# Performance work log

Hardware: AMD Instinct MI355X
Metric: run time of the kernel (lower is better)

Reference implementation:

```python
import jax, jax.numpy as jnp
import numpy as np

SPACE = 63
STRIDE = 2
TEMP = 0.07
W_CHAR, W_WORD, W_PHRASE, W_IDEA = 1.0, 0.5, 0.1, 0.1


def setup_inputs() -> dict:
    key = jax.random.key(0)
    ks = jax.random.split(key, 6)
    B, S, V, D = 8, 4096, 256, 512
    return {
        "logits": jax.random.normal(ks[0], (B, S, V), jnp.float32),
        "word_preds": jax.random.normal(ks[1], (B, D, S // STRIDE), jnp.float32),
        "char_features": jax.random.normal(ks[2], (B, D, S), jnp.float32),
        "contrastive_2": jax.random.normal(ks[3], (B, 128, 1024), jnp.float32),
        "contrastive_3": jax.random.normal(ks[4], (B, 128, 256), jnp.float32),
        "targets": jax.random.randint(ks[5], (B, S), 0, V, jnp.int32),
        "mask": jnp.ones((B, S), jnp.float32),
    }


def _info_nce(emb, temp=TEMP):
    # emb: (B, dim, L). Anchors = even positions, positives = odd positions.
    B, dim, L = emb.shape
    n_pairs = L // 2
    a = emb[:, :, 0:2 * n_pairs:2].transpose(0, 2, 1).reshape(-1, dim)
    p = emb[:, :, 1:2 * n_pairs:2].transpose(0, 2, 1).reshape(-1, dim)
    a = a / jnp.maximum(jnp.linalg.norm(a, axis=1, keepdims=True), 1e-12)
    p = p / jnp.maximum(jnp.linalg.norm(p, axis=1, keepdims=True), 1e-12)
    logits = (a @ p.T) / temp  # (n, n)
    n = logits.shape[0]
    logp = jax.nn.log_softmax(logits, axis=1)
    idx = jnp.arange(n)
    return -jnp.mean(logp[idx, idx])


def _word_span_loss(word_preds, char_features, targets, stride=STRIDE):
    # Segment-mean over spans between consecutive spaces; MSE vs gathered preds.
    B, D, S = char_features.shape
    Wlen = word_preds.shape[2]
    nseg = S + 2  # segment k in [1, n_spaces-1] = span after the k-th space; last slot = junk
    space = targets == SPACE
    cs = jnp.cumsum(space.astype(jnp.int32), axis=1)  # inclusive space count
    seg = jnp.where(space, nseg - 1, cs)          # non-space chars -> span id
    seg_sp = jnp.where(space, cs, nseg - 1)       # space positions -> their space index k
    t_idx = jnp.arange(S, dtype=jnp.int32)

    def per_batch(feats, seg_b, seg_sp_b):
        sums = jax.ops.segment_sum(feats.T, seg_b, num_segments=nseg)  # (nseg, D)
        cnts = jax.ops.segment_sum(jnp.ones((S,), feats.dtype), seg_b, num_segments=nseg)
        pos = jnp.full((nseg,), S, jnp.int32).at[seg_sp_b].set(t_idx)  # position of k-th space
        return sums, cnts, pos

    sums, cnts, pos = jax.vmap(per_batch)(char_features, seg, seg_sp)
    n_sp = cs[:, -1]  # (B,)
    k = jnp.arange(nseg)[None, :]
    valid = (k >= 1) & (k <= n_sp[:, None] - 1) & (cnts > 0) & ((pos // stride) < Wlen)
    means = jax.lax.stop_gradient(sums / jnp.maximum(cnts, 1.0)[..., None])  # target.detach()
    wp = jnp.clip(pos // stride, 0, Wlen - 1)  # (B, nseg)
    preds = jnp.take_along_axis(word_preds.transpose(0, 2, 1), wp[:, :, None], axis=1)  # (B,nseg,D)
    mse = jnp.mean((preds - means) ** 2, axis=-1)  # per-span F.mse_loss (mean over feat dim)
    tot = jnp.sum(jnp.where(valid, mse, 0.0))
    cnt = jnp.sum(valid).astype(mse.dtype)
    return jnp.where(cnt > 0, tot / jnp.maximum(cnt, 1.0), 0.0)


def reference(logits, word_preds, char_features, contrastive_2, contrastive_3, targets, mask):
    # char CE with mask
    logp = jax.nn.log_softmax(logits, axis=-1)
    ce = -jnp.take_along_axis(logp, targets[..., None].astype(jnp.int32), axis=-1)[..., 0]
    n = jnp.sum(mask)
    char_loss = jnp.where(n > 0, jnp.sum(ce * mask) / jnp.maximum(n, 1.0), jnp.mean(ce))
    word_loss = _word_span_loss(word_preds, char_features, targets)
    phrase_loss = _info_nce(contrastive_2)
    idea_loss = _info_nce(contrastive_3)
    return (W_CHAR * char_loss + W_WORD * word_loss
            + W_PHRASE * phrase_loss + W_IDEA * idea_loss)
```

## Files before the change

### kernel.cpp

```cpp
#include <hip/hip_runtime.h>

#define SPACE_TOK 63
#define INV_T 14.285714285714286f
#define SA_SCALE 20.609929155556595f
#define LN2F 0.6931471805599453f

typedef __attribute__((ext_vector_type(8))) short bf16x8;
typedef __attribute__((ext_vector_type(4))) float f32x4;

#define O_NSP    0
#define O_SPPOS  64
#define O_CECM   131136
#define O_CEM    135232
#define O_CEC    139328
#define O_WPART  143424
#define O_WCNT   159808
#define O_NP2    160832
#define O_NP3    161856
#define O_A2     162304
#define SZ_A2    (4096*128*2)
#define O_P2     (O_A2 + SZ_A2)
#define O_A3     (O_P2 + SZ_A2)
#define SZ_A3    (1024*128*2)
#define O_P3     (O_A3 + SZ_A3)

__device__ inline unsigned short f2bf(float x) {
  union { float f; unsigned int u; } c; c.f = x;
  unsigned int r = c.u + 0x7fffu + ((c.u >> 16) & 1u);
  return (unsigned short)(r >> 16);
}

__device__ void scan_body(char* smem, const int* __restrict__ targets, char* ws, int b) {
  int tid = threadIdx.x;
  int* toks = (int*)smem;
  int* sc   = (int*)(smem + 16384);
  int* n_sp   = (int*)(ws + O_NSP);
  int* sp_pos = (int*)(ws + O_SPPOS);
  const int4* tb4 = (const int4*)(targets + b * 4096);
#pragma unroll
  for (int i = 0; i < 4; ++i) ((int4*)toks)[tid + 256 * i] = tb4[tid + 256 * i];
  __syncthreads();
  int base = tid * 16;
  int cnt = 0;
#pragma unroll
  for (int i = 0; i < 16; ++i) cnt += (toks[base + i] == SPACE_TOK);
  sc[tid] = cnt;
  __syncthreads();
  for (int off = 1; off < 256; off <<= 1) {
    int v = (tid >= off) ? sc[tid - off] : 0;
    __syncthreads();
    sc[tid] += v;
    __syncthreads();
  }
  int k = sc[tid] - cnt;
  for (int i = 0; i < 16; ++i)
    if (toks[base + i] == SPACE_TOK) sp_pos[b * 4096 + (k++)] = base + i;
  if (tid == 255) n_sp[b] = sc[255];
}

__device__ void norm_body(char* smem, const float* __restrict__ emb, int L,
                          unsigned short* __restrict__ Abf, unsigned short* __restrict__ Pbf,
                          int b, int l0) {
  float (*tile)[65] = (float(*)[65])smem;
  float (*np4)[64]  = (float(*)[64])(smem + 33280);
  float* scl        = (float*)(smem + 33280 + 1024);
  int tid = threadIdx.x;
  int lx = tid & 63, cq = tid >> 6;
  const float* eb = emb + (size_t)b * 128 * L + l0;
  for (int c = cq; c < 128; c += 4) tile[c][lx] = eb[(size_t)c * L + lx];
  __syncthreads();
  {
    float s = 0.f;
    for (int c = cq; c < 128; c += 4) { float x = tile[c][lx]; s += x * x; }
    np4[cq][lx] = s;
  }
  __syncthreads();
  if (tid < 64) {
    float t = np4[0][tid] + np4[1][tid] + np4[2][tid] + np4[3][tid];
    float nrm = fmaxf(sqrtf(t), 1e-12f);
    scl[tid] = ((tid & 1) ? 1.0f : SA_SCALE) / nrm;
  }
  __syncthreads();
  int c = tid & 127, lh = tid >> 7;
  int half = L >> 1;
  for (int lp = lh; lp < 64; lp += 2) {
    int l = l0 + lp;
    int row = b * half + (l >> 1);
    unsigned short v = f2bf(tile[c][lp] * scl[lp]);
    ((l & 1) ? Pbf : Abf)[(size_t)row * 128 + c] = v;
  }
}

__device__ void ce_body(char* smem, const float* __restrict__ logits,
                        const int* __restrict__ targets, const float* __restrict__ mask,
                        char* ws, int cb) {
  int tid = threadIdx.x;
  int wave = tid >> 6, lane = tid & 63;
  int rbase = cb * 32 + wave * 8;
  float4 v[8];
  float mk[8];
  int tg[8];
#pragma unroll
  for (int rr = 0; rr < 8; ++rr) v[rr] = ((const float4*)logits)[(size_t)(rbase + rr) * 64 + lane];
#pragma unroll
  for (int rr = 0; rr < 8; ++rr) { tg[rr] = targets[rbase + rr]; mk[rr] = mask[rbase + rr]; }
  float aCM = 0.f, aM = 0.f, aC = 0.f;
#pragma unroll
  for (int rr = 0; rr < 8; ++rr) {
    float e = __expf(v[rr].x) + __expf(v[rr].y) + __expf(v[rr].z) + __expf(v[rr].w);
#pragma unroll
    for (int m = 1; m < 64; m <<= 1) e += __shfl_xor(e, m);
    int t = tg[rr];
    int q = t & 3;
    float sel = (q == 0) ? v[rr].x : (q == 1) ? v[rr].y : (q == 2) ? v[rr].z : v[rr].w;
    float xt = __shfl(sel, t >> 2);
    float ce = __logf(e) - xt;
    aCM += ce * mk[rr]; aM += mk[rr]; aC += ce;
  }
  float (*red)[3] = (float(*)[3])smem;
  if (lane == 0) { red[wave][0] = aCM; red[wave][1] = aM; red[wave][2] = aC; }
  __syncthreads();
  if (tid == 0) {
    ((float*)(ws + O_CECM))[cb] = red[0][0] + red[1][0] + red[2][0] + red[3][0];
    ((float*)(ws + O_CEM ))[cb] = red[0][1] + red[1][1] + red[2][1] + red[3][1];
    ((float*)(ws + O_CEC ))[cb] = red[0][2] + red[1][2] + red[2][2] + red[3][2];
  }
}

__global__ void __launch_bounds__(256) fusedA_kernel(const float* __restrict__ logits,
                                                     const int* __restrict__ targets,
                                                     const float* __restrict__ mask,
                                                     const float* __restrict__ c2,
                                                     const float* __restrict__ c3,
                                                     char* __restrict__ ws) {
  extern __shared__ char smem[];
  int bid = blockIdx.x;
  if (bid < 8) {
    scan_body(smem, targets, ws, bid);
  } else if (bid < 136) {
    int nb = bid - 8;
    norm_body(smem, c2, 1024, (unsigned short*)(ws + O_A2), (unsigned short*)(ws + O_P2),
              nb & 7, (nb >> 3) * 64);
  } else if (bid < 168) {
    int nb = bid - 136;
    norm_body(smem, c3, 256, (unsigned short*)(ws + O_A3), (unsigned short*)(ws + O_P3),
              nb & 7, (nb >> 3) * 64);
  } else {
    ce_body(smem, logits, targets, mask, ws, bid - 168);
  }
}

__device__ void nce_body(char* smem, const unsigned short* __restrict__ A,
                         const unsigned short* __restrict__ P, int n,
                         float* __restrict__ slot, int blk) {
  int tid = threadIdx.x;
  int wave = tid >> 6, lane = tid & 63;
  int col = lane & 15, quad = lane >> 4;
  int I0 = blk * 16;
  const unsigned short* Ap = A + (size_t)(I0 + col) * 128 + quad * 8;
  bf16x8 a0 = *(const bf16x8*)(Ap);
  bf16x8 a1 = *(const bf16x8*)(Ap + 32);
  bf16x8 a2 = *(const bf16x8*)(Ap + 64);
  bf16x8 a3 = *(const bf16x8*)(Ap + 96);
  float rl0 = 0.f, rl1 = 0.f, rl2 = 0.f, rl3 = 0.f;
  float dcap = 0.f;
  int Jq = n >> 2;
  int J0w = wave * Jq, Jend = J0w + Jq;
#pragma unroll 2
  for (int J = J0w; J < Jend; J += 16) {
    const unsigned short* Pp = P + (size_t)(J + col) * 128 + quad * 8;
    bf16x8 b0 = *(const bf16x8*)(Pp);
    bf16x8 b1 = *(const bf16x8*)(Pp + 32);
    bf16x8 b2 = *(const bf16x8*)(Pp + 64);
    bf16x8 b3 = *(const bf16x8*)(Pp + 96);
    f32x4 cfr = {0.f, 0.f, 0.f, 0.f};
    cfr = __builtin_amdgcn_mfma_f32_16x16x32_bf16(a0, b0, cfr, 0, 0, 0);
    cfr = __builtin_amdgcn_mfma_f32_16x16x32_bf16(a1, b1, cfr, 0, 0, 0);
    cfr = __builtin_amdgcn_mfma_f32_16x16x32_bf16(a2, b2, cfr, 0, 0, 0);
    cfr = __builtin_amdgcn_mfma_f32_16x16x32_bf16(a3, b3, cfr, 0, 0, 0);
    rl0 += exp2f(cfr[0] - SA_SCALE);
    rl1 += exp2f(cfr[1] - SA_SCALE);
    rl2 += exp2f(cfr[2] - SA_SCALE);
    rl3 += exp2f(cfr[3] - SA_SCALE);
    if (J == I0) {
      int r = col - (quad << 2);
      if (r == 0) dcap = cfr[0];
      else if (r == 1) dcap = cfr[1];
      else if (r == 2) dcap = cfr[2];
      else if (r == 3) dcap = cfr[3];
    }
  }
  float (*part)[16][16] = (float(*)[16][16])smem;
  float (*dpart)[16]    = (float(*)[16])(smem + 4096);
  float* rowc           = (float*)(smem + 4096 + 256);
  part[wave][(quad << 2) + 0][col] = rl0;
  part[wave][(quad << 2) + 1][col] = rl1;
  part[wave][(quad << 2) + 2][col] = rl2;
  part[wave][(quad << 2) + 3][col] = rl3;
  if (quad == (col >> 2)) dpart[wave][col] = dcap;
  __syncthreads();
  {
    int rrow = tid >> 4, cc = tid & 15;
    float s = 0.f, d = 0.f;
#pragma unroll
    for (int w = 0; w < 4; ++w) { s += part[w][rrow][cc]; d += dpart[w][rrow]; }
#pragma unroll
    for (int m = 1; m < 16; m <<= 1) s += __shfl_xor(s, m);
    if (cc == 0) rowc[rrow] = INV_T + __logf(s) - LN2F * d;
  }
  __syncthreads();
  if (tid == 0) {
    float t = 0.f;
#pragma unroll
    for (int i = 0; i < 16; ++i) t += rowc[i];
    *slot = t;
  }
}

__device__ void word_body(char* smem, const float* __restrict__ wp,
                          const float* __restrict__ cf, char* ws, int w) {
  int b = w & 7, y = (w >> 3) & 31, z = w >> 8;
  int ns = ((const int*)(ws + O_NSP))[b];
  const int* sp_pos = (const int*)(ws + O_SPPOS);
  int wave = threadIdx.x >> 6, lane = threadIdx.x & 63;
  int dbase = z * 32 + wave * 8;
  float myacc = 0.f;
  float lcnt = 0.f;
  for (int k = 1 + y; k <= ns - 1; k += 32) {
    int t0 = sp_pos[b * 4096 + k - 1];
    int t1 = sp_pos[b * 4096 + k];
    int cnt = t1 - t0 - 1;
    if (cnt <= 0) continue;
    lcnt += 1.0f;
    int wpos = t0 >> 1;
    float invc = 1.0f / (float)cnt;
    const float* r0 = cf + ((size_t)(b * 512 + dbase)) * 4096;
    int c0 = (t0 + 1) >> 2;
    int c1 = (t1 + 3) >> 2;
    float s0 = 0.f, s1 = 0.f, s2 = 0.f, s3 = 0.f, s4 = 0.f, s5 = 0.f, s6 = 0.f, s7 = 0.f;
    for (int c = c0 + lane; c < c1; c += 64) {
      int tb = c << 2;
      float4 v0 = *(const float4*)(r0 + 0 * 4096 + tb);
      float4 v1 = *(const float4*)(r0 + 1 * 4096 + tb);
      float4 v2 = *(const float4*)(r0 + 2 * 4096 + tb);
      float4 v3 = *(const float4*)(r0 + 3 * 4096 + tb);
      float4 v4 = *(const float4*)(r0 + 4 * 4096 + tb);
      float4 v5 = *(const float4*)(r0 + 5 * 4096 + tb);
      float4 v6 = *(const float4*)(r0 + 6 * 4096 + tb);
      float4 v7 = *(const float4*)(r0 + 7 * 4096 + tb);
      float m0 = (tb + 0 > t0 && tb + 0 < t1) ? 1.f : 0.f;
      float m1 = (tb + 1 > t0 && tb + 1 < t1) ? 1.f : 0.f;
      float m2 = (tb + 2 > t0 && tb + 2 < t1) ? 1.f : 0.f;
      float m3 = (tb + 3 > t0 && tb + 3 < t1) ? 1.f : 0.f;
      s0 += v0.x * m0 + v0.y * m1 + v0.z * m2 + v0.w * m3;
      s1 += v1.x * m0 + v1.y * m1 + v1.z * m2 + v1.w * m3;
      s2 += v2.x * m0 + v2.y * m1 + v2.z * m2 + v2.w * m3;
      s3 += v3.x * m0 + v3.y * m1 + v3.z * m2 + v3.w * m3;
      s4 += v4.x * m0 + v4.y * m1 + v4.z * m2 + v4.w * m3;
      s5 += v5.x * m0 + v5.y * m1 + v5.z * m2 + v5.w * m3;
      s6 += v6.x * m0 + v6.y * m1 + v6.z * m2 + v6.w * m3;
      s7 += v7.x * m0 + v7.y * m1 + v7.z * m2 + v7.w * m3;
    }
#pragma unroll
    for (int m = 1; m < 64; m <<= 1) {
      s0 += __shfl_xor(s0, m); s1 += __shfl_xor(s1, m);
      s2 += __shfl_xor(s2, m); s3 += __shfl_xor(s3, m);
      s4 += __shfl_xor(s4, m); s5 += __shfl_xor(s5, m);
      s6 += __shfl_xor(s6, m); s7 += __shfl_xor(s7, m);
    }
    if (lane < 8) {
      float sv = (lane == 0) ? s0 : (lane == 1) ? s1 : (lane == 2) ? s2 : (lane == 3) ? s3
               : (lane == 4) ? s4 : (lane == 5) ? s5 : (lane == 6) ? s6 : s7;
      float mean = sv * invc;
      float pred = wp[((size_t)(b * 512 + dbase + lane)) * 2048 + wpos];
      float diff = pred - mean;
      myacc += diff * diff;
    }
  }
#pragma unroll
  for (int m = 1; m < 8; m <<= 1) myacc += __shfl_xor(myacc, m);
  float* wacc = (float*)smem;
  if (lane == 0) wacc[wave] = myacc;
  __syncthreads();
  if (threadIdx.x == 0) {
    ((float*)(ws + O_WPART))[w] = (wacc[0] + wacc[1] + wacc[2] + wacc[3]) * (1.0f / 512.0f);
    if (z == 0) ((float*)(ws + O_WCNT))[w] = lcnt;
  }
}

__global__ void __launch_bounds__(256) fusedB_kernel(const float* __restrict__ wp,
                                                     const float* __restrict__ cf,
                                                     char* __restrict__ ws) {
  extern __shared__ char smem[];
  int bid = blockIdx.x;
  if (bid < 256) {
    nce_body(smem, (const unsigned short*)(ws + O_A2), (const unsigned short*)(ws + O_P2),
             4096, (float*)(ws + O_NP2) + bid, bid);
  } else if (bid < 320) {
    int nb = bid - 256;
    nce_body(smem, (const unsigned short*)(ws + O_A3), (const unsigned short*)(ws + O_P3),
             1024, (float*)(ws + O_NP3) + nb, nb);
  } else {
    word_body(smem, wp, cf, ws, bid - 320);
  }
}

__global__ void __launch_bounds__(256) final_kernel(const char* __restrict__ ws,
                                                    float* __restrict__ out) {
  int tid = threadIdx.x;
  int wave = tid >> 6, lane = tid & 63;
  const float* cecm  = (const float*)(ws + O_CECM);
  const float* cem   = (const float*)(ws + O_CEM);
  const float* cec   = (const float*)(ws + O_CEC);
  const float* wpart = (const float*)(ws + O_WPART);
  const float* wcnt  = (const float*)(ws + O_WCNT);
  const float* np2   = (const float*)(ws + O_NP2);
  const float* np3   = (const float*)(ws + O_NP3);
  float v[7] = {0.f, 0.f, 0.f, 0.f, 0.f, 0.f, 0.f};
  for (int i = tid; i < 1024; i += 256) { v[0] += cecm[i]; v[1] += cem[i]; v[2] += cec[i]; }
  for (int i = tid; i < 4096; i += 256) v[3] += wpart[i];
  v[4] = wcnt[tid];
  v[5] = np2[tid];
  if (tid < 64) v[6] = np3[tid];
#pragma unroll
  for (int j = 0; j < 7; ++j) {
    float x = v[j];
#pragma unroll
    for (int m = 1; m < 64; m <<= 1) x += __shfl_xor(x, m);
    v[j] = x;
  }
  __shared__ float fr[4][7];
  if (lane == 0)
#pragma unroll
    for (int j = 0; j < 7; ++j) fr[wave][j] = v[j];
  __syncthreads();
  if (tid == 0) {
    float s[7];
#pragma unroll
    for (int j = 0; j < 7; ++j) s[j] = fr[0][j] + fr[1][j] + fr[2][j] + fr[3][j];
    float n = s[1];
    float charL = (n > 0.f) ? (s[0] / fmaxf(n, 1.f)) : (s[2] / 32768.0f);
    float wordL = (s[4] > 0.f) ? (s[3] / fmaxf(s[4], 1.f)) : 0.f;
    out[0] = charL + 0.5f * wordL + 0.1f * (s[5] / 4096.0f) + 0.1f * (s[6] / 1024.0f);
  }
}

extern "C" void kernel_launch(void* const* d_in, const int* in_sizes, int n_in,
                              void* d_out, int out_size, void* d_ws, size_t ws_size,
                              hipStream_t stream) {
  (void)in_sizes; (void)n_in; (void)out_size; (void)ws_size;
  const float* logits        = (const float*)d_in[0];
  const float* word_preds    = (const float*)d_in[1];
  const float* char_features = (const float*)d_in[2];
  const float* c2            = (const float*)d_in[3];
  const float* c3            = (const float*)d_in[4];
  const int*   targets       = (const int*)d_in[5];
  const float* mask          = (const float*)d_in[6];
  float* out = (float*)d_out;
  char* ws = (char*)d_ws;

  fusedA_kernel<<<1192, 256, 34816, stream>>>(logits, targets, mask, c2, c3, ws);
  fusedB_kernel<<<4416, 256, 4480, stream>>>(word_preds, char_features, ws);
  final_kernel<<<1, 256, 0, stream>>>(ws, out);
}
```

Before: 197.6 us.

## Split InfoNCE column range across 8 blocks and shrink norm tiles

The InfoNCE row-block work is now split across 8 column slices per 16-row block. Each block writes partial exp-sums and diagonal values to the workspace, and the final kernel combines them with the log step. The norm stage now uses 32-column tiles, which doubles its block count and cuts shared memory per block from about 34KB to 18KB. The aim is more parallelism and occupancy in the MFMA-heavy NCE phase and in fusedA, at the cost of extra workspace traffic and more serial work in the single-block final kernel.

```diff
diff --git a/kernel.cpp b/kernel.cpp
--- a/kernel.cpp
+++ b/kernel.cpp
@@ -15,15 +15,19 @@
 #define O_CEC    139328
 #define O_WPART  143424
 #define O_WCNT   159808
-#define O_NP2    160832
-#define O_NP3    161856
-#define O_A2     162304
+#define O_PEXP2  160832
+#define O_PEXP3  291904
+#define O_DIAG2  324672
+#define O_DIAG3  341056
+#define O_A2     345152
 #define SZ_A2    (4096*128*2)
 #define O_P2     (O_A2 + SZ_A2)
 #define O_A3     (O_P2 + SZ_A2)
 #define SZ_A3    (1024*128*2)
 #define O_P3     (O_A3 + SZ_A3)
 
+#define SMEM_A 18048
+
 __device__ inline unsigned short f2bf(float x) {
   union { float f; unsigned int u; } c; c.f = x;
   unsigned int r = c.u + 0x7fffu + ((c.u >> 16) & 1u);
@@ -61,29 +65,31 @@
 __device__ void norm_body(char* smem, const float* __restrict__ emb, int L,
                           unsigned short* __restrict__ Abf, unsigned short* __restrict__ Pbf,
                           int b, int l0) {
-  float (*tile)[65] = (float(*)[65])smem;
-  float (*np4)[64]  = (float(*)[64])(smem + 33280);
-  float* scl        = (float*)(smem + 33280 + 1024);
-  int tid = threadIdx.x;
-  int lx = tid & 63, cq = tid >> 6;
+  float (*tile)[33] = (float(*)[33])smem;
+  float (*np8)[32]  = (float(*)[32])(smem + 16896);
+  float* scl        = (float*)(smem + 16896 + 1024);
+  int tid = threadIdx.x;
+  int lx = tid & 31, cq = tid >> 5;
   const float* eb = emb + (size_t)b * 128 * L + l0;
-  for (int c = cq; c < 128; c += 4) tile[c][lx] = eb[(size_t)c * L + lx];
+  for (int c = cq; c < 128; c += 8) tile[c][lx] = eb[(size_t)c * L + lx];
   __syncthreads();
   {
     float s = 0.f;
-    for (int c = cq; c < 128; c += 4) { float x = tile[c][lx]; s += x * x; }
-    np4[cq][lx] = s;
-  }
-  __syncthreads();
-  if (tid < 64) {
-    float t = np4[0][tid] + np4[1][tid] + np4[2][tid] + np4[3][tid];
+    for (int c = cq; c < 128; c += 8) { float x = tile[c][lx]; s += x * x; }
+    np8[cq][lx] = s;
+  }
+  __syncthreads();
+  if (tid < 32) {
+    float t = 0.f;
+#pragma unroll
+    for (int g = 0; g < 8; ++g) t += np8[g][tid];
     float nrm = fmaxf(sqrtf(t), 1e-12f);
     scl[tid] = ((tid & 1) ? 1.0f : SA_SCALE) / nrm;
   }
   __syncthreads();
   int c = tid & 127, lh = tid >> 7;
   int half = L >> 1;
-  for (int lp = lh; lp < 64; lp += 2) {
+  for (int lp = lh; lp < 32; lp += 2) {
     int l = l0 + lp;
     int row = b * half + (l >> 1);
     unsigned short v = f2bf(tile[c][lp] * scl[lp]);
@@ -137,26 +143,27 @@
   int bid = blockIdx.x;
   if (bid < 8) {
     scan_body(smem, targets, ws, bid);
-  } else if (bid < 136) {
+  } else if (bid < 264) {
     int nb = bid - 8;
     norm_body(smem, c2, 1024, (unsigned short*)(ws + O_A2), (unsigned short*)(ws + O_P2),
-              nb & 7, (nb >> 3) * 64);
-  } else if (bid < 168) {
-    int nb = bid - 136;
+              nb & 7, (nb >> 3) * 32);
+  } else if (bid < 328) {
+    int nb = bid - 264;
     norm_body(smem, c3, 256, (unsigned short*)(ws + O_A3), (unsigned short*)(ws + O_P3),
-              nb & 7, (nb >> 3) * 64);
+              nb & 7, (nb >> 3) * 32);
   } else {
-    ce_body(smem, logits, targets, mask, ws, bid - 168);
+    ce_body(smem, logits, targets, mask, ws, bid - 328);
   }
 }
 
 __device__ void nce_body(char* smem, const unsigned short* __restrict__ A,
-                         const unsigned short* __restrict__ P, int n,
-                         float* __restrict__ slot, int blk) {
+                         const unsigned short* __restrict__ P, int n, int sliceJ,
+                         int blk_i, int s, float* __restrict__ pexp,
+                         float* __restrict__ diag) {
   int tid = threadIdx.x;
   int wave = tid >> 6, lane = tid & 63;
   int col = lane & 15, quad = lane >> 4;
-  int I0 = blk * 16;
+  int I0 = blk_i * 16;
   const unsigned short* Ap = A + (size_t)(I0 + col) * 128 + quad * 8;
   bf16x8 a0 = *(const bf16x8*)(Ap);
   bf16x8 a1 = *(const bf16x8*)(Ap + 32);
@@ -164,8 +171,8 @@
   bf16x8 a3 = *(const bf16x8*)(Ap + 96);
   float rl0 = 0.f, rl1 = 0.f, rl2 = 0.f, rl3 = 0.f;
   float dcap = 0.f;
-  int Jq = n >> 2;
-  int J0w = wave * Jq, Jend = J0w + Jq;
+  int perW = sliceJ >> 2;
+  int J0w = s * sliceJ + wave * perW, Jend = J0w + perW;
 #pragma unroll 2
   for (int J = J0w; J < Jend; J += 16) {
     const unsigned short* Pp = P + (size_t)(J + col) * 128 + quad * 8;
@@ -192,7 +199,6 @@
   }
   float (*part)[16][16] = (float(*)[16][16])smem;
   float (*dpart)[16]    = (float(*)[16])(smem + 4096);
-  float* rowc           = (float*)(smem + 4096 + 256);
   part[wave][(quad << 2) + 0][col] = rl0;
   part[wave][(quad << 2) + 1][col] = rl1;
   part[wave][(quad << 2) + 2][col] = rl2;
@@ -201,19 +207,15 @@
   __syncthreads();
   {
     int rrow = tid >> 4, cc = tid & 15;
-    float s = 0.f, d = 0.f;
-#pragma unroll
-    for (int w = 0; w < 4; ++w) { s += part[w][rrow][cc]; d += dpart[w][rrow]; }
-#pragma unroll
-    for (int m = 1; m < 16; m <<= 1) s += __shfl_xor(s, m);
-    if (cc == 0) rowc[rrow] = INV_T + __logf(s) - LN2F * d;
-  }
-  __syncthreads();
-  if (tid == 0) {
-    float t = 0.f;
-#pragma unroll
-    for (int i = 0; i < 16; ++i) t += rowc[i];
-    *slot = t;
+    float sv = 0.f, d = 0.f;
+#pragma unroll
+    for (int w = 0; w < 4; ++w) { sv += part[w][rrow][cc]; d += dpart[w][rrow]; }
+#pragma unroll
+    for (int m = 1; m < 16; m <<= 1) sv += __shfl_xor(sv, m);
+    if (cc == 0) {
+      pexp[I0 + rrow] = sv;
+      if (I0 >= s * sliceJ && I0 < (s + 1) * sliceJ) diag[I0 + rrow] = d;
+    }
   }
 }
 
@@ -293,15 +295,17 @@
                                                      char* __restrict__ ws) {
   extern __shared__ char smem[];
   int bid = blockIdx.x;
-  if (bid < 256) {
+  if (bid < 2048) {
     nce_body(smem, (const unsigned short*)(ws + O_A2), (const unsigned short*)(ws + O_P2),
-             4096, (float*)(ws + O_NP2) + bid, bid);
-  } else if (bid < 320) {
-    int nb = bid - 256;
+             4096, 512, bid >> 3, bid & 7,
+             (float*)(ws + O_PEXP2) + (bid & 7) * 4096, (float*)(ws + O_DIAG2));
+  } else if (bid < 2560) {
+    int nb = bid - 2048;
     nce_body(smem, (const unsigned short*)(ws + O_A3), (const unsigned short*)(ws + O_P3),
-             1024, (float*)(ws + O_NP3) + nb, nb);
+             1024, 128, nb >> 3, nb & 7,
+             (float*)(ws + O_PEXP3) + (nb & 7) * 1024, (float*)(ws + O_DIAG3));
   } else {
-    word_body(smem, wp, cf, ws, bid - 320);
+    word_body(smem, wp, cf, ws, bid - 2560);
   }
 }
 
@@ -314,14 +318,26 @@
   const float* cec   = (const float*)(ws + O_CEC);
   const float* wpart = (const float*)(ws + O_WPART);
   const float* wcnt  = (const float*)(ws + O_WCNT);
-  const float* np2   = (const float*)(ws + O_NP2);
-  const float* np3   = (const float*)(ws + O_NP3);
+  const float* p2    = (const float*)(ws + O_PEXP2);
+  const float* p3    = (const float*)(ws + O_PEXP3);
+  const float* dg2   = (const float*)(ws + O_DIAG2);
+  const float* dg3   = (const float*)(ws + O_DIAG3);
   float v[7] = {0.f, 0.f, 0.f, 0.f, 0.f, 0.f, 0.f};
   for (int i = tid; i < 1024; i += 256) { v[0] += cecm[i]; v[1] += cem[i]; v[2] += cec[i]; }
   for (int i = tid; i < 4096; i += 256) v[3] += wpart[i];
   v[4] = wcnt[tid];
-  v[5] = np2[tid];
-  if (tid < 64) v[6] = np3[tid];
+  for (int r = tid; r < 4096; r += 256) {
+    float S = 0.f;
+#pragma unroll
+    for (int s = 0; s < 8; ++s) S += p2[s * 4096 + r];
+    v[5] += INV_T + __logf(S) - LN2F * dg2[r];
+  }
+  for (int r = tid; r < 1024; r += 256) {
+    float S = 0.f;
+#pragma unroll
+    for (int s = 0; s < 8; ++s) S += p3[s * 1024 + r];
+    v[6] += INV_T + __logf(S) - LN2F * dg3[r];
+  }
 #pragma unroll
   for (int j = 0; j < 7; ++j) {
     float x = v[j];
@@ -359,7 +375,7 @@
   float* out = (float*)d_out;
   char* ws = (char*)d_ws;
 
-  fusedA_kernel<<<1192, 256, 34816, stream>>>(logits, targets, mask, c2, c3, ws);
-  fusedB_kernel<<<4416, 256, 4480, stream>>>(word_preds, char_features, ws);
+  fusedA_kernel<<<1352, 256, SMEM_A, stream>>>(logits, targets, mask, c2, c3, ws);
+  fusedB_kernel<<<6656, 256, 4480, stream>>>(word_preds, char_features, ws);
   final_kernel<<<1, 256, 0, stream>>>(ws, out);
 }
```

Result: slower. 215.9 us (+9.3%).
